# Kernel optimization log

Measured on AMD Instinct MI355X. Metric: run time of the kernel, lower is better.

## Reference

```python
import jax, jax.numpy as jnp
import numpy as np

NA, NB, NG = 100000, 400000, 5000
IN, OUT, H = 128, 128, 2
SLOPE = 0.2
BN_EPS = 1e-5


def setup_inputs() -> dict:
    key = jax.random.key(0)
    ks = jax.random.split(key, 12)
    return {
        "atom_feats": jax.random.normal(ks[0], (NA, IN), jnp.float32),
        "bond_feats": jax.random.normal(ks[1], (NB, IN), jnp.float32),
        "global_feats": jax.random.normal(ks[2], (NG, IN), jnp.float32),
        "W_atom": jax.random.normal(ks[3], (IN, OUT * H), jnp.float32) * 0.05,
        "W_bond": jax.random.normal(ks[4], (IN, OUT * H), jnp.float32) * 0.05,
        "W_global": jax.random.normal(ks[5], (IN, OUT * H), jnp.float32) * 0.05,
        "attn_l": jax.random.normal(ks[6], (1, H, OUT), jnp.float32) * 0.1,
        "attn_r": jax.random.normal(ks[7], (1, H, OUT), jnp.float32) * 0.1,
        "bn_gamma": jnp.ones((OUT,), jnp.float32),
        "bn_beta": jnp.zeros((OUT,), jnp.float32),
        "src": jax.random.randint(ks[8], (NB,), 0, NA, jnp.int32),
        "dst": jax.random.randint(ks[9], (NB,), 0, NA, jnp.int32),
        "gid": jax.random.randint(ks[10], (NA,), 0, NG, jnp.int32),
    }


def _lrelu(x):
    return jnp.where(x >= 0, x, SLOPE * x)


def reference(atom_feats, bond_feats, global_feats, W_atom, W_bond, W_global,
              attn_l, attn_r, bn_gamma, bn_beta, src, dst, gid):
    Na = atom_feats.shape[0]
    # bias-free single-layer MLPs, reshape to [N, heads, out]
    h = (atom_feats @ W_atom).reshape(-1, H, OUT)      # [Na,H,D]
    e = (bond_feats @ W_bond).reshape(-1, H, OUT)      # [Nb,H,D]
    u = (global_feats @ W_global).reshape(-1, H, OUT)  # [Ng,H,D]

    er = (h * attn_r).sum(-1, keepdims=True)    # [Na,H,1]
    el_h = (h * attn_l).sum(-1, keepdims=True)  # [Na,H,1]
    el_e = (e * attn_l).sum(-1, keepdims=True)  # [Nb,H,1]
    el_u = (u * attn_l).sum(-1, keepdims=True)  # [Ng,H,1]

    # raw attention logits
    eh = _lrelu(el_h[src] + er[dst])   # bond: u_add_v  [Nb,H,1]
    ee = _lrelu(el_e + er[dst])        # bond: e_add_v  [Nb,H,1]
    eu = _lrelu(el_u[gid] + er)        # g2a: u_add_v (one edge per atom) [Na,H,1]

    # max-stabilized softmax over all incoming edges (bond eh, bond ee, g2a eu)
    emax_b = jax.ops.segment_max(jnp.maximum(eh, ee), dst, num_segments=Na)
    emax = jnp.maximum(emax_b, eu)     # [Na,H,1]; eu finite -> no -inf

    eh = jnp.exp(eh - emax[dst])
    ee = jnp.exp(ee - emax[dst])
    eu = jnp.exp(eu - emax)

    esum = jax.ops.segment_sum(eh + ee, dst, num_segments=Na) + eu  # [Na,H,1]

    alpha_h = eh / esum[dst]
    alpha_e = ee / esum[dst]
    alpha_u = eu / esum

    # weighted aggregation
    out = jax.ops.segment_sum(h[src] * alpha_h + e * alpha_e, dst, num_segments=Na)
    out = out + u[gid] * alpha_u       # [Na,H,D]

    hm = out.mean(axis=1)              # mean over heads -> [Na,D]

    # BatchNorm1d (training-mode batch statistics)
    mean = hm.mean(axis=0)
    var = hm.var(axis=0)
    hn = (hm - mean) / jnp.sqrt(var + BN_EPS) * bn_gamma + bn_beta
    return jax.nn.relu(hn)
```

## Files before the change

kernel.cpp:

```cpp
#include <hip/hip_runtime.h>
#include <hip/hip_bf16.h>
#include <cstdint>

typedef __attribute__((ext_vector_type(8))) short bf16x8;
typedef __attribute__((ext_vector_type(4))) float f32x4;

__device__ __forceinline__ float bf2f(unsigned short u) {
    return __uint_as_float(((unsigned)u) << 16);
}
__device__ __forceinline__ unsigned short f2bf(float x) {
    unsigned u = __float_as_uint(x);
    u += 0x7fffu + ((u >> 16) & 1u);
    return (unsigned short)(u >> 16);
}
__device__ __forceinline__ float lrelu(float x) { return x >= 0.f ? x : 0.2f * x; }

__global__ void packW(const float* __restrict__ W, unsigned short* __restrict__ Wp) {
    int idx = blockIdx.x * 256 + threadIdx.x;
    int k = idx >> 8, n = idx & 255;
    int kk = k >> 5, r = k & 31, quad = r >> 3, j = r & 7;
    Wp[(((kk << 8) + n) * 4 + quad) * 8 + j] = f2bf(W[idx]);
}

__global__ __launch_bounds__(256) void gemm_mfma(
    const float* __restrict__ A, const unsigned short* __restrict__ Wp,
    unsigned short* __restrict__ C, int M,
    const float* __restrict__ attn_l, const float* __restrict__ attn_r,
    float* __restrict__ el, float* __restrict__ er)
{
    __shared__ unsigned short lds[16896];
    const int t = threadIdx.x;
    const int row0 = blockIdx.x * 64;

#pragma unroll
    for (int i = 0; i < 8; i++) {
        int flat = i * 4096 + t * 16;
        int row = flat >> 9;
        int colf = (flat & 511) >> 2;
        float4 v = make_float4(0.f, 0.f, 0.f, 0.f);
        if (row0 + row < M) v = *(const float4*)(A + (size_t)(row0 + row) * 128 + colf);
        unsigned u0 = (unsigned)f2bf(v.x) | ((unsigned)f2bf(v.y) << 16);
        unsigned u1 = (unsigned)f2bf(v.z) | ((unsigned)f2bf(v.w) << 16);
        *(uint2*)(&lds[row * 136 + colf]) = make_uint2(u0, u1);
    }
    __syncthreads();

    const int w = t >> 6, lane = t & 63;
    const int quad = lane >> 4, l16 = lane & 15;
    const int col0w = w * 64;

    f32x4 acc[4][4];
#pragma unroll
    for (int rt = 0; rt < 4; rt++)
#pragma unroll
        for (int ct = 0; ct < 4; ct++) acc[rt][ct] = (f32x4)(0.f);

#pragma unroll
    for (int kk = 0; kk < 4; kk++) {
        bf16x8 af[4], bf[4];
#pragma unroll
        for (int rt = 0; rt < 4; rt++)
            af[rt] = *(const bf16x8*)(&lds[(rt * 16 + l16) * 136 + kk * 32 + quad * 8]);
#pragma unroll
        for (int ct = 0; ct < 4; ct++) {
            int n = col0w + ct * 16 + l16;
            bf[ct] = *(const bf16x8*)(Wp + ((((kk << 8) + n) * 4 + quad) << 3));
        }
#pragma unroll
        for (int rt = 0; rt < 4; rt++)
#pragma unroll
            for (int ct = 0; ct < 4; ct++)
                acc[rt][ct] = __builtin_amdgcn_mfma_f32_16x16x32_bf16(af[rt], bf[ct], acc[rt][ct], 0, 0, 0);
    }
    __syncthreads();

#pragma unroll
    for (int rt = 0; rt < 4; rt++)
#pragma unroll
        for (int ct = 0; ct < 4; ct++) {
#pragma unroll
            for (int r = 0; r < 4; r++) {
                int row = rt * 16 + quad * 4 + r;
                int col = col0w + ct * 16 + l16;
                lds[row * 264 + col] = f2bf(acc[rt][ct][r]);
            }
        }
    __syncthreads();

#pragma unroll
    for (int i = 0; i < 8; i++) {
        int flat = i * 4096 + t * 16;
        int row = flat >> 9;
        int cb = flat & 511;
        uint4 v = *(const uint4*)((const char*)lds + row * 528 + cb);
        int grow = row0 + row;
        bool valid = grow < M;
        if (valid) *(uint4*)((char*)C + (size_t)grow * 512 + cb) = v;

        int ch = cb >> 1;
        float x0 = bf2f((unsigned short)(v.x & 0xffff)), x1 = bf2f((unsigned short)(v.x >> 16));
        float x2 = bf2f((unsigned short)(v.y & 0xffff)), x3 = bf2f((unsigned short)(v.y >> 16));
        float x4 = bf2f((unsigned short)(v.z & 0xffff)), x5 = bf2f((unsigned short)(v.z >> 16));
        float x6 = bf2f((unsigned short)(v.w & 0xffff)), x7 = bf2f((unsigned short)(v.w >> 16));
        float4 al0 = *(const float4*)(attn_l + ch);
        float4 al1 = *(const float4*)(attn_l + ch + 4);
        float dl = x0 * al0.x + x1 * al0.y + x2 * al0.z + x3 * al0.w
                 + x4 * al1.x + x5 * al1.y + x6 * al1.z + x7 * al1.w;
        float dr = 0.f;
        if (er) {
            float4 ar0 = *(const float4*)(attn_r + ch);
            float4 ar1 = *(const float4*)(attn_r + ch + 4);
            dr = x0 * ar0.x + x1 * ar0.y + x2 * ar0.z + x3 * ar0.w
               + x4 * ar1.x + x5 * ar1.y + x6 * ar1.z + x7 * ar1.w;
        }
#pragma unroll
        for (int off = 8; off >= 1; off >>= 1) {
            dl += __shfl_xor(dl, off);
            dr += __shfl_xor(dr, off);
        }
        if ((t & 15) == 0 && valid) {
            int head = (ch >> 7) & 1;
            el[(size_t)grow * 2 + head] = dl;
            if (er) er[(size_t)grow * 2 + head] = dr;
        }
    }
}

__global__ void hist_kernel(const int* __restrict__ dst, int* __restrict__ deg, int Nb) {
    int t = blockIdx.x * blockDim.x + threadIdx.x;
    if (t < Nb) atomicAdd(&deg[dst[t]], 1);
}

__global__ __launch_bounds__(1024) void scan1024(
    const int* __restrict__ deg, int* __restrict__ rowptr, int* __restrict__ wo, int n)
{
    __shared__ int wsum[16];
    int t = threadIdx.x, lane = t & 63, w = t >> 6;
    int carry = 0;
    for (int base = 0; base < n; base += 1024) {
        int i = base + t;
        int v = (i < n) ? deg[i] : 0;
        int x = v;
#pragma unroll
        for (int off = 1; off < 64; off <<= 1) {
            int y = __shfl_up(x, off);
            if (lane >= off) x += y;
        }
        if (lane == 63) wsum[w] = x;
        __syncthreads();
        if (w == 0) {
            int s = (lane < 16) ? wsum[lane] : 0;
#pragma unroll
            for (int off = 1; off < 16; off <<= 1) {
                int y = __shfl_up(s, off);
                if (lane >= off) s += y;
            }
            if (lane < 16) wsum[lane] = s;
        }
        __syncthreads();
        int wofs = (w > 0) ? wsum[w - 1] : 0;
        int incl = carry + wofs + x;
        if (i < n) { rowptr[i + 1] = incl; wo[i] = incl - v; }
        int total = wsum[15];
        __syncthreads();
        carry += total;
    }
    if (t == 0) rowptr[0] = 0;
}

__global__ void fill_kernel(const int* __restrict__ src, const int* __restrict__ dst,
                            const float* __restrict__ er, const float* __restrict__ elh,
                            const float* __restrict__ ele,
                            int* __restrict__ wo, int* __restrict__ sidx,
                            int* __restrict__ eidx, float4* __restrict__ logits, int Nb) {
    int t = blockIdx.x * blockDim.x + threadIdx.x;
    if (t >= Nb) return;
    int d = dst[t], s = src[t];
    int p = atomicAdd(&wo[d], 1);
    float e0 = er[(size_t)d * 2], e1 = er[(size_t)d * 2 + 1];
    float h0 = elh[(size_t)s * 2], h1 = elh[(size_t)s * 2 + 1];
    float l0 = ele[(size_t)t * 2], l1 = ele[(size_t)t * 2 + 1];
    sidx[p] = s;
    eidx[p] = t;
    logits[p] = make_float4(lrelu(h0 + e0), lrelu(h1 + e1), lrelu(l0 + e0), lrelu(l1 + e1));
}

__global__ __launch_bounds__(256) void aggregate(
    const unsigned short* __restrict__ h, const unsigned short* __restrict__ e,
    const unsigned short* __restrict__ u,
    const float* __restrict__ er, const float* __restrict__ elu,
    const int* __restrict__ rowptr, const int* __restrict__ sidx,
    const int* __restrict__ eidx, const float4* __restrict__ logits,
    const int* __restrict__ gid,
    float* __restrict__ hm, int Na)
{
    int wid = (int)((blockIdx.x * (unsigned)blockDim.x + threadIdx.x) >> 6);
    int lane = threadIdx.x & 63;
    if (wid >= Na) return;
    const int a = wid;
    const float er0 = er[(size_t)a * 2], er1 = er[(size_t)a * 2 + 1];
    const int g = gid[a];
    const float eul0 = lrelu(elu[(size_t)g * 2] + er0);
    const float eul1 = lrelu(elu[(size_t)g * 2 + 1] + er1);
    const int rb = rowptr[a], re = rowptr[a + 1];

    float m0 = eul0, m1 = eul1;
    for (int base = rb; base < re; base += 64) {
        int i = base + lane;
        float lm0 = -1e30f, lm1 = -1e30f;
        if (i < re) {
            float4 lg = logits[i];
            lm0 = fmaxf(lg.x, lg.z);
            lm1 = fmaxf(lg.y, lg.w);
        }
#pragma unroll
        for (int off = 32; off >= 1; off >>= 1) {
            lm0 = fmaxf(lm0, __shfl_xor(lm0, off));
            lm1 = fmaxf(lm1, __shfl_xor(lm1, off));
        }
        m0 = fmaxf(m0, lm0);
        m1 = fmaxf(m1, lm1);
    }

    float es0 = __expf(eul0 - m0), es1 = __expf(eul1 - m1);
    const int head = lane >> 5;
    const int d4 = lane << 2;
    float acc0, acc1, acc2, acc3;
    {
        float eu_sel = head ? es1 : es0;
        ushort4 uv = *(const ushort4*)(u + (size_t)g * 256 + d4);
        acc0 = eu_sel * bf2f(uv.x); acc1 = eu_sel * bf2f(uv.y);
        acc2 = eu_sel * bf2f(uv.z); acc3 = eu_sel * bf2f(uv.w);
    }

    for (int base = rb; base < re; base += 64) {
        int n = min(64, re - base);
        float xh0 = 0.f, xh1 = 0.f, xe0 = 0.f, xe1 = 0.f;
        int sv = 0, bv = 0;
        if (lane < n) {
            float4 lg = logits[base + lane];
            xh0 = __expf(lg.x - m0); xh1 = __expf(lg.y - m1);
            xe0 = __expf(lg.z - m0); xe1 = __expf(lg.w - m1);
            sv = sidx[base + lane];
            bv = eidx[base + lane];
        }
        float s0 = xh0 + xe0, s1 = xh1 + xe1;
#pragma unroll
        for (int off = 32; off >= 1; off >>= 1) {
            s0 += __shfl_xor(s0, off);
            s1 += __shfl_xor(s1, off);
        }
        es0 += s0; es1 += s1;

        for (int j = 0; j < n; j++) {
            int s_j = __shfl(sv, j), b_j = __shfl(bv, j);
            float wh0 = __shfl(xh0, j), wh1 = __shfl(xh1, j);
            float we0 = __shfl(xe0, j), we1 = __shfl(xe1, j);
            float wh = head ? wh1 : wh0;
            float we = head ? we1 : we0;
            ushort4 hv = *(const ushort4*)(h + (size_t)s_j * 256 + d4);
            ushort4 ev = *(const ushort4*)(e + (size_t)b_j * 256 + d4);
            acc0 += wh * bf2f(hv.x) + we * bf2f(ev.x);
            acc1 += wh * bf2f(hv.y) + we * bf2f(ev.y);
            acc2 += wh * bf2f(hv.z) + we * bf2f(ev.z);
            acc3 += wh * bf2f(hv.w) + we * bf2f(ev.w);
        }
    }

    float inv = 1.f / (head ? es1 : es0);
    acc0 *= inv; acc1 *= inv; acc2 *= inv; acc3 *= inv;
    float p0 = __shfl(acc0, (lane + 32) & 63);
    float p1 = __shfl(acc1, (lane + 32) & 63);
    float p2 = __shfl(acc2, (lane + 32) & 63);
    float p3 = __shfl(acc3, (lane + 32) & 63);
    if (lane < 32) {
        float4 o = make_float4(0.5f * (acc0 + p0), 0.5f * (acc1 + p1),
                               0.5f * (acc2 + p2), 0.5f * (acc3 + p3));
        *(float4*)(hm + (size_t)a * 128 + d4) = o;
    }
}

__global__ void bnstats(const float* __restrict__ hm, float* __restrict__ sums, int Na) {
    int t = threadIdx.x;
    int c = t & 127, half = t >> 7;
    float s = 0.f, ss = 0.f;
    for (int r = blockIdx.x * 2 + half; r < Na; r += gridDim.x * 2) {
        float v = hm[(size_t)r * 128 + c];
        s += v; ss += v * v;
    }
    atomicAdd(&sums[c], s);
    atomicAdd(&sums[128 + c], ss);
}

__global__ void bnapply(const float* __restrict__ hm, const float* __restrict__ sums,
                        const float* __restrict__ gamma, const float* __restrict__ beta,
                        float* __restrict__ out, int Na) {
    int t = threadIdx.x;
    int c = t & 127, half = t >> 7;
    float invn = 1.f / (float)Na;
    float mean = sums[c] * invn;
    float var = sums[128 + c] * invn - mean * mean;
    float scale = gamma[c] * rsqrtf(var + 1e-5f);
    float shift = beta[c] - mean * scale;
    for (int r = blockIdx.x * 2 + half; r < Na; r += gridDim.x * 2) {
        float v = hm[(size_t)r * 128 + c] * scale + shift;
        out[(size_t)r * 128 + c] = fmaxf(v, 0.f);
    }
}

extern "C" void kernel_launch(void* const* d_in, const int* in_sizes, int n_in,
                              void* d_out, int out_size, void* d_ws, size_t ws_size,
                              hipStream_t stream)
{
    const float* atom   = (const float*)d_in[0];
    const float* bondf  = (const float*)d_in[1];
    const float* globf  = (const float*)d_in[2];
    const float* Wa     = (const float*)d_in[3];
    const float* Wb     = (const float*)d_in[4];
    const float* Wg     = (const float*)d_in[5];
    const float* attn_l = (const float*)d_in[6];
    const float* attn_r = (const float*)d_in[7];
    const float* gamma  = (const float*)d_in[8];
    const float* beta   = (const float*)d_in[9];
    const int* src      = (const int*)d_in[10];
    const int* dst      = (const int*)d_in[11];
    const int* gid      = (const int*)d_in[12];
    const int Na = in_sizes[0] / 128;
    const int Nb = in_sizes[1] / 128;
    const int Ng = in_sizes[2] / 128;

    char* w = (char*)d_ws;
    size_t off = 0;
    auto alloc = [&](size_t bytes) -> void* {
        void* p = w + off;
        off = (off + bytes + 255) & ~(size_t)255;
        return p;
    };
    unsigned short* h   = (unsigned short*)alloc((size_t)Na * 256 * 2);
    unsigned short* e   = (unsigned short*)alloc((size_t)Nb * 256 * 2);
    unsigned short* u   = (unsigned short*)alloc((size_t)Ng * 256 * 2);
    unsigned short* Wpa = (unsigned short*)alloc(32768 * 2);
    unsigned short* Wpb = (unsigned short*)alloc(32768 * 2);
    unsigned short* Wpg = (unsigned short*)alloc(32768 * 2);
    float* er   = (float*)alloc((size_t)Na * 2 * 4);
    float* elh  = (float*)alloc((size_t)Na * 2 * 4);
    float* ele  = (float*)alloc((size_t)Nb * 2 * 4);
    float* elu  = (float*)alloc((size_t)Ng * 2 * 4);
    int* deg    = (int*)alloc((size_t)Na * 4);
    int* rowptr = (int*)alloc((size_t)(Na + 1) * 4);
    int* wo     = (int*)alloc((size_t)Na * 4);
    int* sidx   = (int*)alloc((size_t)Nb * 4);
    int* eidx   = (int*)alloc((size_t)Nb * 4);
    float4* logits = (float4*)alloc((size_t)Nb * 16);
    float* hm   = (float*)alloc((size_t)Na * 128 * 4);
    float* sums = (float*)alloc(256 * 4);

    hipMemsetAsync(deg, 0, (size_t)Na * 4, stream);
    hipMemsetAsync(sums, 0, 256 * 4, stream);

    packW<<<128, 256, 0, stream>>>(Wa, Wpa);
    packW<<<128, 256, 0, stream>>>(Wb, Wpb);
    packW<<<128, 256, 0, stream>>>(Wg, Wpg);

    gemm_mfma<<<(Na + 63) / 64, 256, 0, stream>>>(atom, Wpa, h, Na, attn_l, attn_r, elh, er);
    gemm_mfma<<<(Nb + 63) / 64, 256, 0, stream>>>(bondf, Wpb, e, Nb, attn_l, nullptr, ele, nullptr);
    gemm_mfma<<<(Ng + 63) / 64, 256, 0, stream>>>(globf, Wpg, u, Ng, attn_l, nullptr, elu, nullptr);

    hist_kernel<<<(Nb + 255) / 256, 256, 0, stream>>>(dst, deg, Nb);
    scan1024<<<1, 1024, 0, stream>>>(deg, rowptr, wo, Na);
    fill_kernel<<<(Nb + 255) / 256, 256, 0, stream>>>(src, dst, er, elh, ele,
                                                      wo, sidx, eidx, logits, Nb);

    aggregate<<<(Na + 3) / 4, 256, 0, stream>>>(h, e, u, er, elu,
                                                rowptr, sidx, eidx, logits, gid, hm, Na);
    bnstats<<<256, 256, 0, stream>>>(hm, sums, Na);
    bnapply<<<512, 256, 0, stream>>>(hm, sums, gamma, beta, (float*)d_out, Na);
}
```

Baseline: 817.7 us.

## Fold attention vectors into weights, load GEMM A directly to registers, vectorize scan

A new kernel precomputes W·attn_l and W·attn_r per input channel, so el/er come from the fp32 inputs as a dot product computed inside the GEMM K loop instead of from the bf16 outputs afterward. The GEMM now loads A fragments straight from global memory into registers, dropping the LDS staging pass and one barrier. It also gains a tail-specialized template and a launch-bounds occupancy hint. The single-block scan handles four elements per thread with int4 loads, which cuts its serial iterations. The cost is uncoalesced-ish strided global loads for A and slightly different numerics, since the logits are now taken from fp32 inputs rather than rounded bf16 outputs.

```diff
diff --git a/kernel.cpp b/kernel.cpp
--- a/kernel.cpp
+++ b/kernel.cpp
@@ -22,29 +22,35 @@
     Wp[(((kk << 8) + n) * 4 + quad) * 8 + j] = f2bf(W[idx]);
 }
 
-__global__ __launch_bounds__(256) void gemm_mfma(
+__global__ void makeV(const float* __restrict__ W, const float* __restrict__ al,
+                      const float* __restrict__ ar, float* __restrict__ vv) {
+    int t = threadIdx.x;
+    int k = t >> 1, h = t & 1;
+    const float* wp = W + k * 256 + h * 128;
+    const float* alp = al + h * 128;
+    const float* arp = ar + h * 128;
+    float sl = 0.f, sr = 0.f;
+#pragma unroll
+    for (int d = 0; d < 128; d += 4) {
+        float4 wv = *(const float4*)(wp + d);
+        float4 av = *(const float4*)(alp + d);
+        float4 rv = *(const float4*)(arp + d);
+        sl += wv.x * av.x + wv.y * av.y + wv.z * av.z + wv.w * av.w;
+        sr += wv.x * rv.x + wv.y * rv.y + wv.z * rv.z + wv.w * rv.w;
+    }
+    vv[k * 4 + h] = sl;
+    vv[k * 4 + 2 + h] = sr;
+}
+
+template<bool TAIL>
+__device__ __forceinline__ void gemm_body(
     const float* __restrict__ A, const unsigned short* __restrict__ Wp,
     unsigned short* __restrict__ C, int M,
-    const float* __restrict__ attn_l, const float* __restrict__ attn_r,
-    float* __restrict__ el, float* __restrict__ er)
+    const float4* __restrict__ vv,
+    float* __restrict__ el, float* __restrict__ er,
+    unsigned short* lds, int row0)
 {
-    __shared__ unsigned short lds[16896];
     const int t = threadIdx.x;
-    const int row0 = blockIdx.x * 64;
-
-#pragma unroll
-    for (int i = 0; i < 8; i++) {
-        int flat = i * 4096 + t * 16;
-        int row = flat >> 9;
-        int colf = (flat & 511) >> 2;
-        float4 v = make_float4(0.f, 0.f, 0.f, 0.f);
-        if (row0 + row < M) v = *(const float4*)(A + (size_t)(row0 + row) * 128 + colf);
-        unsigned u0 = (unsigned)f2bf(v.x) | ((unsigned)f2bf(v.y) << 16);
-        unsigned u1 = (unsigned)f2bf(v.z) | ((unsigned)f2bf(v.w) << 16);
-        *(uint2*)(&lds[row * 136 + colf]) = make_uint2(u0, u1);
-    }
-    __syncthreads();
-
     const int w = t >> 6, lane = t & 63;
     const int quad = lane >> 4, l16 = lane & 15;
     const int col0w = w * 64;
@@ -55,36 +61,80 @@
 #pragma unroll
         for (int ct = 0; ct < 4; ct++) acc[rt][ct] = (f32x4)(0.f);
 
+    float dl0 = 0.f, dl1 = 0.f, dr0 = 0.f, dr1 = 0.f;
+
 #pragma unroll
     for (int kk = 0; kk < 4; kk++) {
-        bf16x8 af[4], bf[4];
-#pragma unroll
-        for (int rt = 0; rt < 4; rt++)
-            af[rt] = *(const bf16x8*)(&lds[(rt * 16 + l16) * 136 + kk * 32 + quad * 8]);
+        bf16x8 bfr[4];
 #pragma unroll
         for (int ct = 0; ct < 4; ct++) {
             int n = col0w + ct * 16 + l16;
-            bf[ct] = *(const bf16x8*)(Wp + ((((kk << 8) + n) * 4 + quad) << 3));
-        }
-#pragma unroll
-        for (int rt = 0; rt < 4; rt++)
+            bfr[ct] = *(const bf16x8*)(Wp + ((((kk << 8) + n) * 4 + quad) << 3));
+        }
+        float4 fa[4][2];
+#pragma unroll
+        for (int rt = 0; rt < 4; rt++) {
+            int row = row0 + rt * 16 + l16;
+            if (!TAIL || row < M) {
+                const float* ap = A + (size_t)row * 128 + kk * 32 + quad * 8;
+                fa[rt][0] = *(const float4*)ap;
+                fa[rt][1] = *(const float4*)(ap + 4);
+            } else {
+                fa[rt][0] = make_float4(0.f, 0.f, 0.f, 0.f);
+                fa[rt][1] = make_float4(0.f, 0.f, 0.f, 0.f);
+            }
+        }
+#pragma unroll
+        for (int rt = 0; rt < 4; rt++) {
+            if (w == rt) {
+                const float4* vp = vv + kk * 32 + quad * 8;
+                float x0 = fa[rt][0].x, x1 = fa[rt][0].y, x2 = fa[rt][0].z, x3 = fa[rt][0].w;
+                float x4 = fa[rt][1].x, x5 = fa[rt][1].y, x6 = fa[rt][1].z, x7 = fa[rt][1].w;
+                float4 c0 = vp[0], c1 = vp[1], c2 = vp[2], c3 = vp[3];
+                float4 c4 = vp[4], c5 = vp[5], c6 = vp[6], c7 = vp[7];
+                dl0 += x0*c0.x + x1*c1.x + x2*c2.x + x3*c3.x + x4*c4.x + x5*c5.x + x6*c6.x + x7*c7.x;
+                dl1 += x0*c0.y + x1*c1.y + x2*c2.y + x3*c3.y + x4*c4.y + x5*c5.y + x6*c6.y + x7*c7.y;
+                dr0 += x0*c0.z + x1*c1.z + x2*c2.z + x3*c3.z + x4*c4.z + x5*c5.z + x6*c6.z + x7*c7.z;
+                dr1 += x0*c0.w + x1*c1.w + x2*c2.w + x3*c3.w + x4*c4.w + x5*c5.w + x6*c6.w + x7*c7.w;
+            }
+            bf16x8 af;
+            af[0] = (short)f2bf(fa[rt][0].x);
+            af[1] = (short)f2bf(fa[rt][0].y);
+            af[2] = (short)f2bf(fa[rt][0].z);
+            af[3] = (short)f2bf(fa[rt][0].w);
+            af[4] = (short)f2bf(fa[rt][1].x);
+            af[5] = (short)f2bf(fa[rt][1].y);
+            af[6] = (short)f2bf(fa[rt][1].z);
+            af[7] = (short)f2bf(fa[rt][1].w);
 #pragma unroll
             for (int ct = 0; ct < 4; ct++)
-                acc[rt][ct] = __builtin_amdgcn_mfma_f32_16x16x32_bf16(af[rt], bf[ct], acc[rt][ct], 0, 0, 0);
-    }
-    __syncthreads();
+                acc[rt][ct] = __builtin_amdgcn_mfma_f32_16x16x32_bf16(af, bfr[ct], acc[rt][ct], 0, 0, 0);
+        }
+    }
+
+    dl0 += __shfl_xor(dl0, 16); dl0 += __shfl_xor(dl0, 32);
+    dl1 += __shfl_xor(dl1, 16); dl1 += __shfl_xor(dl1, 32);
+    dr0 += __shfl_xor(dr0, 16); dr0 += __shfl_xor(dr0, 32);
+    dr1 += __shfl_xor(dr1, 16); dr1 += __shfl_xor(dr1, 32);
+    {
+        int drow = row0 + w * 16 + l16;
+        if (!TAIL || drow < M) {
+            if (quad == 0) el[(size_t)drow * 2] = dl0;
+            else if (quad == 1) el[(size_t)drow * 2 + 1] = dl1;
+            else if (er) {
+                if (quad == 2) er[(size_t)drow * 2] = dr0;
+                else er[(size_t)drow * 2 + 1] = dr1;
+            }
+        }
+    }
 
 #pragma unroll
     for (int rt = 0; rt < 4; rt++)
 #pragma unroll
-        for (int ct = 0; ct < 4; ct++) {
-#pragma unroll
-            for (int r = 0; r < 4; r++) {
-                int row = rt * 16 + quad * 4 + r;
-                int col = col0w + ct * 16 + l16;
-                lds[row * 264 + col] = f2bf(acc[rt][ct][r]);
-            }
-        }
+        for (int ct = 0; ct < 4; ct++)
+#pragma unroll
+            for (int r = 0; r < 4; r++)
+                lds[(rt * 16 + quad * 4 + r) * 264 + col0w + ct * 16 + l16] = f2bf(acc[rt][ct][r]);
     __syncthreads();
 
 #pragma unroll
@@ -92,38 +142,23 @@
         int flat = i * 4096 + t * 16;
         int row = flat >> 9;
         int cb = flat & 511;
-        uint4 v = *(const uint4*)((const char*)lds + row * 528 + cb);
         int grow = row0 + row;
-        bool valid = grow < M;
-        if (valid) *(uint4*)((char*)C + (size_t)grow * 512 + cb) = v;
-
-        int ch = cb >> 1;
-        float x0 = bf2f((unsigned short)(v.x & 0xffff)), x1 = bf2f((unsigned short)(v.x >> 16));
-        float x2 = bf2f((unsigned short)(v.y & 0xffff)), x3 = bf2f((unsigned short)(v.y >> 16));
-        float x4 = bf2f((unsigned short)(v.z & 0xffff)), x5 = bf2f((unsigned short)(v.z >> 16));
-        float x6 = bf2f((unsigned short)(v.w & 0xffff)), x7 = bf2f((unsigned short)(v.w >> 16));
-        float4 al0 = *(const float4*)(attn_l + ch);
-        float4 al1 = *(const float4*)(attn_l + ch + 4);
-        float dl = x0 * al0.x + x1 * al0.y + x2 * al0.z + x3 * al0.w
-                 + x4 * al1.x + x5 * al1.y + x6 * al1.z + x7 * al1.w;
-        float dr = 0.f;
-        if (er) {
-            float4 ar0 = *(const float4*)(attn_r + ch);
-            float4 ar1 = *(const float4*)(attn_r + ch + 4);
-            dr = x0 * ar0.x + x1 * ar0.y + x2 * ar0.z + x3 * ar0.w
-               + x4 * ar1.x + x5 * ar1.y + x6 * ar1.z + x7 * ar1.w;
-        }
-#pragma unroll
-        for (int off = 8; off >= 1; off >>= 1) {
-            dl += __shfl_xor(dl, off);
-            dr += __shfl_xor(dr, off);
-        }
-        if ((t & 15) == 0 && valid) {
-            int head = (ch >> 7) & 1;
-            el[(size_t)grow * 2 + head] = dl;
-            if (er) er[(size_t)grow * 2 + head] = dr;
-        }
-    }
+        if (!TAIL || grow < M)
+            *(uint4*)((char*)C + (size_t)grow * 512 + cb) =
+                *(const uint4*)((const char*)lds + row * 528 + cb);
+    }
+}
+
+__global__ __launch_bounds__(256, 4) void gemm_mfma(
+    const float* __restrict__ A, const unsigned short* __restrict__ Wp,
+    unsigned short* __restrict__ C, int M,
+    const float4* __restrict__ vv,
+    float* __restrict__ el, float* __restrict__ er)
+{
+    __shared__ unsigned short lds[16896];
+    int row0 = blockIdx.x * 64;
+    if (row0 + 64 <= M) gemm_body<false>(A, Wp, C, M, vv, el, er, lds, row0);
+    else                gemm_body<true >(A, Wp, C, M, vv, el, er, lds, row0);
 }
 
 __global__ void hist_kernel(const int* __restrict__ dst, int* __restrict__ deg, int Nb) {
@@ -131,16 +166,24 @@
     if (t < Nb) atomicAdd(&deg[dst[t]], 1);
 }
 
-__global__ __launch_bounds__(1024) void scan1024(
+__global__ __launch_bounds__(1024) void scan4096(
     const int* __restrict__ deg, int* __restrict__ rowptr, int* __restrict__ wo, int n)
 {
     __shared__ int wsum[16];
     int t = threadIdx.x, lane = t & 63, w = t >> 6;
     int carry = 0;
-    for (int base = 0; base < n; base += 1024) {
-        int i = base + t;
-        int v = (i < n) ? deg[i] : 0;
-        int x = v;
+    for (int base = 0; base < n; base += 4096) {
+        int i0 = base + t * 4;
+        int4 v = make_int4(0, 0, 0, 0);
+        if (i0 + 3 < n) v = *(const int4*)(deg + i0);
+        else {
+            if (i0 < n)     v.x = deg[i0];
+            if (i0 + 1 < n) v.y = deg[i0 + 1];
+            if (i0 + 2 < n) v.z = deg[i0 + 2];
+            if (i0 + 3 < n) v.w = deg[i0 + 3];
+        }
+        int tsum = v.x + v.y + v.z + v.w;
+        int x = tsum;
 #pragma unroll
         for (int off = 1; off < 64; off <<= 1) {
             int y = __shfl_up(x, off);
@@ -159,9 +202,13 @@
         }
         __syncthreads();
         int wofs = (w > 0) ? wsum[w - 1] : 0;
-        int incl = carry + wofs + x;
-        if (i < n) { rowptr[i + 1] = incl; wo[i] = incl - v; }
         int total = wsum[15];
+        int e0 = carry + wofs + (x - tsum);
+        int e1 = e0 + v.x, e2 = e1 + v.y, e3 = e2 + v.z;
+        if (i0 < n)     { wo[i0]     = e0; rowptr[i0 + 1] = e1; }
+        if (i0 + 1 < n) { wo[i0 + 1] = e1; rowptr[i0 + 2] = e2; }
+        if (i0 + 2 < n) { wo[i0 + 2] = e2; rowptr[i0 + 3] = e3; }
+        if (i0 + 3 < n) { wo[i0 + 3] = e3; rowptr[i0 + 4] = e3 + v.w; }
         __syncthreads();
         carry += total;
     }
@@ -342,6 +389,9 @@
     unsigned short* Wpa = (unsigned short*)alloc(32768 * 2);
     unsigned short* Wpb = (unsigned short*)alloc(32768 * 2);
     unsigned short* Wpg = (unsigned short*)alloc(32768 * 2);
+    float* vva  = (float*)alloc(512 * 4);
+    float* vvb  = (float*)alloc(512 * 4);
+    float* vvg  = (float*)alloc(512 * 4);
     float* er   = (float*)alloc((size_t)Na * 2 * 4);
     float* elh  = (float*)alloc((size_t)Na * 2 * 4);
     float* ele  = (float*)alloc((size_t)Nb * 2 * 4);
@@ -361,13 +411,16 @@
     packW<<<128, 256, 0, stream>>>(Wa, Wpa);
     packW<<<128, 256, 0, stream>>>(Wb, Wpb);
     packW<<<128, 256, 0, stream>>>(Wg, Wpg);
-
-    gemm_mfma<<<(Na + 63) / 64, 256, 0, stream>>>(atom, Wpa, h, Na, attn_l, attn_r, elh, er);
-    gemm_mfma<<<(Nb + 63) / 64, 256, 0, stream>>>(bondf, Wpb, e, Nb, attn_l, nullptr, ele, nullptr);
-    gemm_mfma<<<(Ng + 63) / 64, 256, 0, stream>>>(globf, Wpg, u, Ng, attn_l, nullptr, elu, nullptr);
+    makeV<<<1, 256, 0, stream>>>(Wa, attn_l, attn_r, vva);
+    makeV<<<1, 256, 0, stream>>>(Wb, attn_l, attn_r, vvb);
+    makeV<<<1, 256, 0, stream>>>(Wg, attn_l, attn_r, vvg);
+
+    gemm_mfma<<<(Na + 63) / 64, 256, 0, stream>>>(atom, Wpa, h, Na, (const float4*)vva, elh, er);
+    gemm_mfma<<<(Nb + 63) / 64, 256, 0, stream>>>(bondf, Wpb, e, Nb, (const float4*)vvb, ele, nullptr);
+    gemm_mfma<<<(Ng + 63) / 64, 256, 0, stream>>>(globf, Wpg, u, Ng, (const float4*)vvg, elu, nullptr);
 
     hist_kernel<<<(Nb + 255) / 256, 256, 0, stream>>>(dst, deg, Nb);
-    scan1024<<<1, 1024, 0, stream>>>(deg, rowptr, wo, Na);
+    scan4096<<<1, 1024, 0, stream>>>(deg, rowptr, wo, Na);
     fill_kernel<<<(Nb + 255) / 256, 256, 0, stream>>>(src, dst, er, elh, ele,
                                                       wo, sidx, eidx, logits, Nb);
 
```

After: 1.162 ms. 42.1% more time.
